# Kernel optimization log

Hardware: AMD Instinct MI355X
Metric: run time of the kernel (lower is better)

Reference implementation:

```python
import jax, jax.numpy as jnp
import numpy as np

N = 50000
E = 640000
NFEAT = 128
NHID = 128
ALPHA = 0.2  # leaky relu slope


def setup_inputs() -> dict:
    key = jax.random.key(0)
    k1, k2, k3, k4, k5 = jax.random.split(key, 5)
    x = jax.random.normal(k1, (N, NFEAT), dtype=jnp.float32)
    W = jax.random.normal(k2, (NFEAT, NHID), dtype=jnp.float32) * (1.0 / np.sqrt(NFEAT))
    a = jax.random.normal(k3, (1, 2 * NHID), dtype=jnp.float32) * 0.1
    # every node appears at least once as a source so rowsum > 0 (as in a real adjacency)
    src = jnp.concatenate([jnp.arange(N, dtype=jnp.int64 if jax.config.read('jax_enable_x64') else jnp.int32),
                           jax.random.randint(k4, (E - N,), 0, N)]).astype(jnp.int32)
    dst = jax.random.randint(k5, (E,), 0, N).astype(jnp.int32)
    edge_index = jnp.stack([src, dst], axis=0)
    return {"x": x, "W": W, "a": a, "edge_index": edge_index, "no_need_param": 0}


def reference(x, W, a, edge_index, no_need_param):
    # SpGraphAttentionLayer (concat=False), single head
    h = x @ W                                   # [N, nhid]
    src, dst = edge_index[0], edge_index[1]     # [E]
    nhid = W.shape[1]
    a1, a2 = a[0, :nhid], a[0, nhid:]
    # a @ cat(h[src], h[dst])  ==  h[src]@a1 + h[dst]@a2
    score = h[src] @ a1 + h[dst] @ a2           # [E]
    e = jnp.exp(-jax.nn.leaky_relu(score, ALPHA))
    n = x.shape[0]
    rowsum = jax.ops.segment_sum(e, src, num_segments=n)              # [N]
    h_prime = jax.ops.segment_sum(e[:, None] * h[dst], src, num_segments=n)  # [N, nhid]
    neighborhood_emb = h_prime / (rowsum[:, None] + 1e-16)
    # fused combine: elu(x @ W - neighborhood aggregation)
    mapped_fea = x @ W
    return jax.nn.elu(mapped_fea - neighborhood_emb)
```

## Files before the change

### kernel.cpp

```cpp
#include <hip/hip_runtime.h>
#include <hip/hip_fp16.h>
#include <math.h>

#define NFEAT 128
#define NHID  128
#define ALPHA 0.2f

typedef __attribute__((ext_vector_type(8))) short short8;
typedef __attribute__((ext_vector_type(4))) float f32x4;

__device__ inline unsigned int pack_bf16x2_rn(float x, float y) {
    unsigned int bx = __float_as_uint(x), by = __float_as_uint(y);
    bx += 0x7fffu + ((bx >> 16) & 1u);
    by += 0x7fffu + ((by >> 16) & 1u);
    return (bx >> 16) | (by & 0xffff0000u);
}

union Frag { unsigned int u[4]; uint4 v; short8 s; };

__global__ __launch_bounds__(256) void prep_wt_kernel(
    const float* __restrict__ W, unsigned int* __restrict__ Wtg,
    int* __restrict__ hist, int n)
{
    const int t = threadIdx.x;

    if (blockIdx.x >= 16) {
        const int n4     = n >> 2;
        const int stride = (gridDim.x - 16) << 8;
        int4* h4 = (int4*)hist;
        for (int i = (blockIdx.x - 16) * 256 + t; i < n4; i += stride)
            h4[i] = make_int4(0, 0, 0, 0);
        for (int i = (n4 << 2) + (blockIdx.x - 16) * 256 + t; i < n; i += stride)
            hist[i] = 0;
        return;
    }

    __shared__ float tile[32][33];
    const int kt = blockIdx.x >> 2;
    const int nt = blockIdx.x & 3;

    {
        const int r = t >> 3, c = t & 7;
        const float4 v = *((const float4*)&W[(size_t)(kt * 32 + r) * NHID + nt * 32 + c * 4]);
        tile[r][c * 4 + 0] = v.x; tile[r][c * 4 + 1] = v.y;
        tile[r][c * 4 + 2] = v.z; tile[r][c * 4 + 3] = v.w;
    }
    __syncthreads();

    const int nn = t & 31;
    #pragma unroll
    for (int i = 0; i < 2; ++i) {
        const int kk = (t >> 5) * 2 + i;
        Wtg[(size_t)(nt * 32 + nn) * 64 + kt * 16 + kk] =
            pack_bf16x2_rn(tile[kk * 2][nn], tile[kk * 2 + 1][nn]);
    }
}

__global__ __launch_bounds__(256) void gemm_h_kernel(
    const float* __restrict__ x, const unsigned int* __restrict__ Wtg,
    const float* __restrict__ a, unsigned int* __restrict__ hbu,
    float* __restrict__ s1, float* __restrict__ s2, int n,
    const int* __restrict__ ei, int* __restrict__ hist, int E, int gemm_blocks)
{
    __shared__ unsigned int Wtu[128 * 64];

    const int t = threadIdx.x;

    if (blockIdx.x >= gemm_blocks) {
        const int E4   = E >> 2;
        const int nthr = (gridDim.x - gemm_blocks) << 8;
        const int g    = (blockIdx.x - gemm_blocks) * 256 + t;
        for (int idx = g; idx < E4; idx += nthr) {
            const int4 s4 = ((const int4*)ei)[idx];
            atomicAdd(&hist[s4.x], 1);
            atomicAdd(&hist[s4.y], 1);
            atomicAdd(&hist[s4.z], 1);
            atomicAdd(&hist[s4.w], 1);
        }
        for (int j = (E4 << 2) + g; j < E; j += nthr) atomicAdd(&hist[ei[j]], 1);
        return;
    }

    #pragma unroll
    for (int i = 0; i < 8; ++i) {
        const int u  = i * 256 + t;
        const uint4 v = ((const uint4*)Wtg)[u];
        const int nn = u >> 4, kc = u & 15;
        *((uint4*)&Wtu[nn * 64 + (kc ^ (nn & 15)) * 4]) = v;
    }

    const int w    = t >> 6;
    const int lane = t & 63;
    const int c    = lane & 15;
    const int quad = lane >> 4;

    const int rowbase = blockIdx.x * 64 + w * 16;

    int arow = rowbase + c; if (arow >= n) arow = n - 1;
    const float4* xp = (const float4*)(x + (size_t)arow * NFEAT);
    float4 xv[8];
    #pragma unroll
    for (int s = 0; s < 4; ++s) {
        xv[2 * s]     = xp[s * 8 + quad * 2];
        xv[2 * s + 1] = xp[s * 8 + quad * 2 + 1];
    }

    float a1v[8], a2v[8];
    #pragma unroll
    for (int tt = 0; tt < 8; ++tt) {
        a1v[tt] = a[tt * 16 + c];
        a2v[tt] = a[NHID + tt * 16 + c];
    }

    f32x4 acc[8];
    #pragma unroll
    for (int tt = 0; tt < 8; ++tt) acc[tt] = (f32x4){0.f, 0.f, 0.f, 0.f};

    __syncthreads();

    #pragma unroll
    for (int s = 0; s < 4; ++s) {
        Frag afr;
        afr.u[0] = pack_bf16x2_rn(xv[2 * s].x,     xv[2 * s].y);
        afr.u[1] = pack_bf16x2_rn(xv[2 * s].z,     xv[2 * s].w);
        afr.u[2] = pack_bf16x2_rn(xv[2 * s + 1].x, xv[2 * s + 1].y);
        afr.u[3] = pack_bf16x2_rn(xv[2 * s + 1].z, xv[2 * s + 1].w);
        const int kc = s * 4 + quad;
        #pragma unroll
        for (int tt = 0; tt < 8; ++tt) {
            Frag bfr;
            bfr.v = *((const uint4*)&Wtu[(tt * 16 + c) * 64 + (kc ^ c) * 4]);
            acc[tt] = __builtin_amdgcn_mfma_f32_16x16x32_bf16(
                afr.s, bfr.s, acc[tt], 0, 0, 0);
        }
    }

    #pragma unroll
    for (int r = 0; r < 4; ++r) {
        const int  row = rowbase + quad * 4 + r;
        const bool ok  = (row < n);
        float p1 = 0.f, p2 = 0.f;
        #pragma unroll
        for (int tt = 0; tt < 8; ++tt) {
            const float v = acc[tt][r];
            p1 = fmaf(v, a1v[tt], p1);
            p2 = fmaf(v, a2v[tt], p2);
        }
        if (ok) {
            uint4 pk;
            pk.x = pack_bf16x2_rn(acc[0][r], acc[1][r]);
            pk.y = pack_bf16x2_rn(acc[2][r], acc[3][r]);
            pk.z = pack_bf16x2_rn(acc[4][r], acc[5][r]);
            pk.w = pack_bf16x2_rn(acc[6][r], acc[7][r]);
            *((uint4*)&hbu[(size_t)row * 64 + c * 4]) = pk;
        }
        #pragma unroll
        for (int off = 1; off <= 8; off <<= 1) {
            p1 += __shfl_xor(p1, off, 64);
            p2 += __shfl_xor(p2, off, 64);
        }
        if (ok && c == 0) { s1[row] = p1; s2[row] = p2; }
    }
}

__global__ __launch_bounds__(256) void scan_block_kernel(
    const int* __restrict__ in, int* __restrict__ out, int* __restrict__ bsums, int n)
{
    __shared__ int s[256];
    const int tid = threadIdx.x;
    const int gid = blockIdx.x * 256 + tid;
    const int v = (gid < n) ? in[gid] : 0;
    s[tid] = v;
    __syncthreads();
    #pragma unroll
    for (int off = 1; off < 256; off <<= 1) {
        const int t2 = (tid >= off) ? s[tid - off] : 0;
        __syncthreads();
        s[tid] += t2;
        __syncthreads();
    }
    if (gid < n) out[gid] = s[tid] - v;
    if (tid == 255) bsums[blockIdx.x] = s[255];
}

__global__ __launch_bounds__(256) void scan_add_kernel(
    int* __restrict__ row_ptr, int* __restrict__ cursor,
    const int* __restrict__ bsums, int n, int E, int nb)
{
    __shared__ int s[256];
    const int tid = threadIdx.x;
    s[tid] = (tid < nb) ? bsums[tid] : 0;
    __syncthreads();
    #pragma unroll
    for (int off = 1; off < 256; off <<= 1) {
        const int t2 = (tid >= off) ? s[tid - off] : 0;
        __syncthreads();
        s[tid] += t2;
        __syncthreads();
    }
    const int offset = (blockIdx.x == 0) ? 0 : s[blockIdx.x - 1];
    const int gid = blockIdx.x * 256 + tid;
    if (gid < n) {
        const int v = row_ptr[gid] + offset;
        row_ptr[gid] = v;
        cursor[gid]  = v;
    }
    if (gid == 0) row_ptr[n] = E;
}

__global__ __launch_bounds__(256) void scatter_kernel(
    const int* __restrict__ ei, const float* __restrict__ s1,
    const float* __restrict__ s2, int* __restrict__ cursor,
    unsigned int* __restrict__ erec, int E)
{
    const int j = blockIdx.x * 256 + threadIdx.x;
    if (j >= E) return;
    const int src = ei[j];
    const int dst = ei[E + j];
    float s = s1[src] + s2[dst];
    s = (s > 0.f) ? s : ALPHA * s;
    const float ev = expf(-s);
    const unsigned int evh = (unsigned int)__half_as_ushort(__float2half(ev));
    const int pos = atomicAdd(&cursor[src], 1);
    erec[pos] = ((unsigned int)dst << 16) | evh;
}

__global__ __launch_bounds__(256) void aggregate_kernel(
    const int* __restrict__ row_ptr, const unsigned int* __restrict__ erec,
    const unsigned int* __restrict__ hbu, float* __restrict__ out, int n)
{
    const int node = (blockIdx.x * 256 + threadIdx.x) >> 4;
    const int l    = threadIdx.x & 15;
    if (node >= n) return;

    const int beg = row_ptr[node];
    const int end = row_ptr[node + 1];

    float acc[8];
    #pragma unroll
    for (int i = 0; i < 8; ++i) acc[i] = 0.f;
    float rs = 0.f;

    const uint4* hbu4 = (const uint4*)hbu;

    #define BL(x) __uint_as_float((x) << 16)
    #define BH(x) __uint_as_float((x) & 0xffff0000u)
    #define ACC4(u, ev)                                   \
        acc[0] = fmaf(ev, BL(u.x), acc[0]);               \
        acc[4] = fmaf(ev, BH(u.x), acc[4]);               \
        acc[1] = fmaf(ev, BL(u.y), acc[1]);               \
        acc[5] = fmaf(ev, BH(u.y), acc[5]);               \
        acc[2] = fmaf(ev, BL(u.z), acc[2]);               \
        acc[6] = fmaf(ev, BH(u.z), acc[6]);               \
        acc[3] = fmaf(ev, BL(u.w), acc[3]);               \
        acc[7] = fmaf(ev, BH(u.w), acc[7]);

    int e = beg;
    for (; e + 8 <= end; e += 8) {
        unsigned int rr[8];
        uint4 u[8];
        #pragma unroll
        for (int i = 0; i < 8; ++i) rr[i] = erec[e + i];
        #pragma unroll
        for (int i = 0; i < 8; ++i)
            u[i] = hbu4[(size_t)(rr[i] >> 16) * 16 + l];
        #pragma unroll
        for (int i = 0; i < 8; ++i) {
            const float ev = __half2float(__ushort_as_half((unsigned short)(rr[i] & 0xffffu)));
            ACC4(u[i], ev);
            rs += ev;
        }
    }
    for (; e + 2 <= end; e += 2) {
        const unsigned int r0 = erec[e], r1 = erec[e + 1];
        const uint4 u0 = hbu4[(size_t)(r0 >> 16) * 16 + l];
        const uint4 u1 = hbu4[(size_t)(r1 >> 16) * 16 + l];
        const float e0 = __half2float(__ushort_as_half((unsigned short)(r0 & 0xffffu)));
        const float e1 = __half2float(__ushort_as_half((unsigned short)(r1 & 0xffffu)));
        ACC4(u0, e0); ACC4(u1, e1);
        rs += e0 + e1;
    }
    if (e < end) {
        const unsigned int r0 = erec[e];
        const uint4 u0 = hbu4[(size_t)(r0 >> 16) * 16 + l];
        const float e0 = __half2float(__ushort_as_half((unsigned short)(r0 & 0xffffu)));
        ACC4(u0, e0);
        rs += e0;
    }
    #undef ACC4

    const float rinv = 1.0f / (rs + 1e-16f);
    const uint4 us = hbu4[(size_t)node * 16 + l];
    float* op = out + (size_t)node * NHID + l;
    float z;
    z = BL(us.x) - acc[0] * rinv; op[0]   = (z > 0.f) ? z : (expf(z) - 1.f);
    z = BH(us.x) - acc[4] * rinv; op[16]  = (z > 0.f) ? z : (expf(z) - 1.f);
    z = BL(us.y) - acc[1] * rinv; op[32]  = (z > 0.f) ? z : (expf(z) - 1.f);
    z = BH(us.y) - acc[5] * rinv; op[48]  = (z > 0.f) ? z : (expf(z) - 1.f);
    z = BL(us.z) - acc[2] * rinv; op[64]  = (z > 0.f) ? z : (expf(z) - 1.f);
    z = BH(us.z) - acc[6] * rinv; op[80]  = (z > 0.f) ? z : (expf(z) - 1.f);
    z = BL(us.w) - acc[3] * rinv; op[96]  = (z > 0.f) ? z : (expf(z) - 1.f);
    z = BH(us.w) - acc[7] * rinv; op[112] = (z > 0.f) ? z : (expf(z) - 1.f);
    #undef BL
    #undef BH
}

extern "C" void kernel_launch(void* const* d_in, const int* in_sizes, int n_in,
                              void* d_out, int out_size, void* d_ws, size_t ws_size,
                              hipStream_t stream) {
    const float* x  = (const float*)d_in[0];
    const float* W  = (const float*)d_in[1];
    const float* a  = (const float*)d_in[2];
    const int*   ei = (const int*)d_in[3];

    const int n = in_sizes[0] / NFEAT;
    const int E = in_sizes[3] / 2;
    const int nb = (n + 255) / 256;

    float* out = (float*)d_out;

    unsigned int* hbu    = (unsigned int*)d_ws;
    float*        s1     = (float*)(hbu + (size_t)n * 64);
    float*        s2     = s1 + n;
    unsigned int* erec   = (unsigned int*)(s2 + n);
    unsigned int* Wtg    = erec + E;
    int*          hist   = (int*)(Wtg + 8192);
    int*          bsums  = hist + n;
    int*          row_ptr = bsums + 256;
    int*          cursor  = row_ptr + (n + 1);

    prep_wt_kernel<<<16 + 50, 256, 0, stream>>>(W, Wtg, hist, n);

    const int gemm_blocks = (n + 63) / 64;
    const int hist_blocks = 128;
    gemm_h_kernel<<<gemm_blocks + hist_blocks, 256, 0, stream>>>(
        x, Wtg, a, hbu, s1, s2, n, ei, hist, E, gemm_blocks);

    scan_block_kernel<<<nb, 256, 0, stream>>>(hist, row_ptr, bsums, n);
    scan_add_kernel<<<nb, 256, 0, stream>>>(row_ptr, cursor, bsums, n, E, nb);

    scatter_kernel<<<(E + 255) / 256, 256, 0, stream>>>(ei, s1, s2, cursor, erec, E);

    aggregate_kernel<<<((size_t)n * 16 + 255) / 256, 256, 0, stream>>>(
        row_ptr, erec, hbu, out, n);
}
```

Measured before the change: 176.2 us.

## Fold attention vector into GEMM via W·a and merge scan into single-pass decoupled lookback

Precomputes W·a1 and W·a2 in the prep kernel so the per-node attention scores come from one extra MFMA per k-step. This replaces the per-row FMA reduction and cross-lane shuffles in the GEMM epilogue. The two-kernel block scan plus add is also replaced by one single-pass scan using a ticket counter and decoupled lookback, which removes a launch. In exchange, s1/s2 are now computed from bf16-rounded x and W·a rather than the fp32 accumulator, and the lookback spins on atomics, so blocks can serialize.

Measured after the change: 185.5 us. +5.3%, slower.

```diff
diff --git a/kernel.cpp b/kernel.cpp
--- a/kernel.cpp
+++ b/kernel.cpp
@@ -19,19 +19,27 @@
 union Frag { unsigned int u[4]; uint4 v; short8 s; };
 
 __global__ __launch_bounds__(256) void prep_wt_kernel(
-    const float* __restrict__ W, unsigned int* __restrict__ Wtg,
-    int* __restrict__ hist, int n)
+    const float* __restrict__ W, const float* __restrict__ a,
+    unsigned int* __restrict__ Wtg, float* __restrict__ b12,
+    int* __restrict__ zero_base, int zero_cnt)
 {
     const int t = threadIdx.x;
 
-    if (blockIdx.x >= 16) {
-        const int n4     = n >> 2;
-        const int stride = (gridDim.x - 16) << 8;
-        int4* h4 = (int4*)hist;
-        for (int i = (blockIdx.x - 16) * 256 + t; i < n4; i += stride)
-            h4[i] = make_int4(0, 0, 0, 0);
-        for (int i = (n4 << 2) + (blockIdx.x - 16) * 256 + t; i < n; i += stride)
-            hist[i] = 0;
+    if (blockIdx.x == 16) {
+        const int which = t >> 7;
+        const int k     = t & 127;
+        const float* wr = W + (size_t)k * NHID;
+        const float* av = a + which * NHID;
+        float acc = 0.f;
+        #pragma unroll 8
+        for (int j = 0; j < NHID; ++j) acc = fmaf(wr[j], av[j], acc);
+        b12[which * NHID + k] = acc;
+        return;
+    }
+    if (blockIdx.x > 16) {
+        const int stride = (gridDim.x - 17) << 8;
+        for (int i = (blockIdx.x - 17) * 256 + t; i < zero_cnt; i += stride)
+            zero_base[i] = 0;
         return;
     }
 
@@ -58,7 +66,7 @@
 
 __global__ __launch_bounds__(256) void gemm_h_kernel(
     const float* __restrict__ x, const unsigned int* __restrict__ Wtg,
-    const float* __restrict__ a, unsigned int* __restrict__ hbu,
+    const float* __restrict__ b12, unsigned int* __restrict__ hbu,
     float* __restrict__ s1, float* __restrict__ s2, int n,
     const int* __restrict__ ei, int* __restrict__ hist, int E, int gemm_blocks)
 {
@@ -105,16 +113,24 @@
         xv[2 * s + 1] = xp[s * 8 + quad * 2 + 1];
     }
 
-    float a1v[8], a2v[8];
-    #pragma unroll
-    for (int tt = 0; tt < 8; ++tt) {
-        a1v[tt] = a[tt * 16 + c];
-        a2v[tt] = a[NHID + tt * 16 + c];
+    Frag sfr[4];
+    #pragma unroll
+    for (int s = 0; s < 4; ++s) {
+        if (c < 2) {
+            const float* bp = b12 + c * NHID + s * 32 + quad * 8;
+            sfr[s].u[0] = pack_bf16x2_rn(bp[0], bp[1]);
+            sfr[s].u[1] = pack_bf16x2_rn(bp[2], bp[3]);
+            sfr[s].u[2] = pack_bf16x2_rn(bp[4], bp[5]);
+            sfr[s].u[3] = pack_bf16x2_rn(bp[6], bp[7]);
+        } else {
+            sfr[s].u[0] = 0; sfr[s].u[1] = 0; sfr[s].u[2] = 0; sfr[s].u[3] = 0;
+        }
     }
 
     f32x4 acc[8];
     #pragma unroll
     for (int tt = 0; tt < 8; ++tt) acc[tt] = (f32x4){0.f, 0.f, 0.f, 0.f};
+    f32x4 accs = (f32x4){0.f, 0.f, 0.f, 0.f};
 
     __syncthreads();
 
@@ -133,43 +149,41 @@
             acc[tt] = __builtin_amdgcn_mfma_f32_16x16x32_bf16(
                 afr.s, bfr.s, acc[tt], 0, 0, 0);
         }
+        accs = __builtin_amdgcn_mfma_f32_16x16x32_bf16(afr.s, sfr[s].s, accs, 0, 0, 0);
     }
 
     #pragma unroll
     for (int r = 0; r < 4; ++r) {
-        const int  row = rowbase + quad * 4 + r;
-        const bool ok  = (row < n);
-        float p1 = 0.f, p2 = 0.f;
-        #pragma unroll
-        for (int tt = 0; tt < 8; ++tt) {
-            const float v = acc[tt][r];
-            p1 = fmaf(v, a1v[tt], p1);
-            p2 = fmaf(v, a2v[tt], p2);
-        }
-        if (ok) {
+        const int row = rowbase + quad * 4 + r;
+        if (row < n) {
             uint4 pk;
             pk.x = pack_bf16x2_rn(acc[0][r], acc[1][r]);
             pk.y = pack_bf16x2_rn(acc[2][r], acc[3][r]);
             pk.z = pack_bf16x2_rn(acc[4][r], acc[5][r]);
             pk.w = pack_bf16x2_rn(acc[6][r], acc[7][r]);
             *((uint4*)&hbu[(size_t)row * 64 + c * 4]) = pk;
-        }
-        #pragma unroll
-        for (int off = 1; off <= 8; off <<= 1) {
-            p1 += __shfl_xor(p1, off, 64);
-            p2 += __shfl_xor(p2, off, 64);
-        }
-        if (ok && c == 0) { s1[row] = p1; s2[row] = p2; }
-    }
-}
-
-__global__ __launch_bounds__(256) void scan_block_kernel(
-    const int* __restrict__ in, int* __restrict__ out, int* __restrict__ bsums, int n)
+            if (c == 0)      s1[row] = accs[r];
+            else if (c == 1) s2[row] = accs[r];
+        }
+    }
+}
+
+__global__ __launch_bounds__(256) void scan_onepass_kernel(
+    const int* __restrict__ hist, unsigned long long* __restrict__ pscan,
+    int* __restrict__ tcounter, int* __restrict__ row_ptr,
+    int* __restrict__ cursor, int n, int E)
 {
     __shared__ int s[256];
+    __shared__ int sb;
+    __shared__ int sprefix;
     const int tid = threadIdx.x;
-    const int gid = blockIdx.x * 256 + tid;
-    const int v = (gid < n) ? in[gid] : 0;
+
+    if (tid == 0) sb = atomicAdd(tcounter, 1);
+    __syncthreads();
+    const int b   = sb;
+    const int gid = b * 256 + tid;
+
+    const int v = (gid < n) ? hist[gid] : 0;
     s[tid] = v;
     __syncthreads();
     #pragma unroll
@@ -179,31 +193,31 @@
         s[tid] += t2;
         __syncthreads();
     }
-    if (gid < n) out[gid] = s[tid] - v;
-    if (tid == 255) bsums[blockIdx.x] = s[255];
-}
-
-__global__ __launch_bounds__(256) void scan_add_kernel(
-    int* __restrict__ row_ptr, int* __restrict__ cursor,
-    const int* __restrict__ bsums, int n, int E, int nb)
-{
-    __shared__ int s[256];
-    const int tid = threadIdx.x;
-    s[tid] = (tid < nb) ? bsums[tid] : 0;
-    __syncthreads();
-    #pragma unroll
-    for (int off = 1; off < 256; off <<= 1) {
-        const int t2 = (tid >= off) ? s[tid - off] : 0;
-        __syncthreads();
-        s[tid] += t2;
-        __syncthreads();
-    }
-    const int offset = (blockIdx.x == 0) ? 0 : s[blockIdx.x - 1];
-    const int gid = blockIdx.x * 256 + tid;
+    const int total = s[255];
+
+    if (tid == 0) {
+        if (b == 0) {
+            atomicExch(&pscan[0], (2ULL << 32) | (unsigned int)total);
+            sprefix = 0;
+        } else {
+            atomicExch(&pscan[b], (1ULL << 32) | (unsigned int)total);
+            int running = 0;
+            for (int i = b - 1; i >= 0; --i) {
+                unsigned long long p;
+                do { p = atomicAdd(&pscan[i], 0ULL); } while ((p >> 32) == 0ULL);
+                running += (int)(unsigned int)p;
+                if ((p >> 32) == 2ULL) break;
+            }
+            atomicExch(&pscan[b], (2ULL << 32) | (unsigned int)(running + total));
+            sprefix = running;
+        }
+    }
+    __syncthreads();
+
     if (gid < n) {
-        const int v = row_ptr[gid] + offset;
-        row_ptr[gid] = v;
-        cursor[gid]  = v;
+        const int val = s[tid] - v + sprefix;
+        row_ptr[gid] = val;
+        cursor[gid]  = val;
     }
     if (gid == 0) row_ptr[n] = E;
 }
@@ -319,25 +333,28 @@
 
     float* out = (float*)d_out;
 
-    unsigned int* hbu    = (unsigned int*)d_ws;
-    float*        s1     = (float*)(hbu + (size_t)n * 64);
-    float*        s2     = s1 + n;
-    unsigned int* erec   = (unsigned int*)(s2 + n);
-    unsigned int* Wtg    = erec + E;
-    int*          hist   = (int*)(Wtg + 8192);
-    int*          bsums  = hist + n;
-    int*          row_ptr = bsums + 256;
-    int*          cursor  = row_ptr + (n + 1);
-
-    prep_wt_kernel<<<16 + 50, 256, 0, stream>>>(W, Wtg, hist, n);
+    unsigned int*       hbu     = (unsigned int*)d_ws;
+    float*              s1      = (float*)(hbu + (size_t)n * 64);
+    float*              s2      = s1 + n;
+    unsigned int*       erec    = (unsigned int*)(s2 + n);
+    unsigned int*       Wtg     = erec + E;
+    float*              b12     = (float*)(Wtg + 8192);
+    int*                hist    = (int*)(b12 + 256);
+    unsigned long long* pscan   = (unsigned long long*)(hist + n);
+    int*                tcounter = (int*)(pscan + 256);
+    int*                row_ptr  = tcounter + 2;
+    int*                cursor   = row_ptr + (n + 1);
+
+    prep_wt_kernel<<<16 + 1 + 49, 256, 0, stream>>>(W, a, Wtg, b12,
+                                                    hist, n + 514);
 
     const int gemm_blocks = (n + 63) / 64;
     const int hist_blocks = 128;
     gemm_h_kernel<<<gemm_blocks + hist_blocks, 256, 0, stream>>>(
-        x, Wtg, a, hbu, s1, s2, n, ei, hist, E, gemm_blocks);
-
-    scan_block_kernel<<<nb, 256, 0, stream>>>(hist, row_ptr, bsums, n);
-    scan_add_kernel<<<nb, 256, 0, stream>>>(row_ptr, cursor, bsums, n, E, nb);
+        x, Wtg, b12, hbu, s1, s2, n, ei, hist, E, gemm_blocks);
+
+    scan_onepass_kernel<<<nb, 256, 0, stream>>>(hist, pscan, tcounter,
+                                                row_ptr, cursor, n, E);
 
     scatter_kernel<<<(E + 255) / 256, 256, 0, stream>>>(ei, s1, s2, cursor, erec, E);
 
```
